# Optimization experiments

Hardware: AMD Instinct MI355X
Metric: run time of the kernel (lower is better)

The kernel has to match this reference:

```python
import jax, jax.numpy as jnp
import numpy as np

K = 1024
D = 64
BETA = 0.25
EPS = 1e-10


def setup_inputs() -> dict:
    key = jax.random.key(0)
    k1, k2 = jax.random.split(key)
    z = jax.random.normal(k1, (64, D, 32, 32), dtype=jnp.float32)
    # embedding.weight.data.uniform_(-1/K, 1/K)
    emb = jax.random.uniform(k2, (K, D), dtype=jnp.float32,
                             minval=-1.0 / K, maxval=1.0 / K)
    return {"z": z, "emb": emb}


def reference(z, emb):
    sg = jax.lax.stop_gradient
    B, C, H, W = z.shape  # C == D
    zp = jnp.transpose(z, (0, 2, 3, 1))            # [B,H,W,D]
    zf = zp.reshape(-1, C)                          # [N,D]
    # squared-euclidean distances via matmul (cdist expansion)
    d = (jnp.sum(zf ** 2, axis=1, keepdims=True)
         + jnp.sum(emb ** 2, axis=1)
         - 2.0 * jnp.matmul(zf, emb.T))             # [N,K]
    idx = jnp.argmin(d, axis=1)                     # [N] int
    z_q = emb[idx].reshape(zp.shape)                # gather == one-hot matmul
    loss = (jnp.mean((sg(z_q) - zp) ** 2)
            + BETA * jnp.mean((z_q - sg(zp)) ** 2))
    # straight-through estimator
    z_q_st = zp + sg(z_q - zp)
    # codebook usage perplexity
    n = zf.shape[0]
    e_mean = jnp.zeros((K,), dtype=zf.dtype).at[idx].add(1.0) / n
    perplexity = jnp.exp(-jnp.sum(e_mean * jnp.log(e_mean + EPS)))
    z_q_out = jnp.transpose(z_q_st, (0, 3, 1, 2))   # back to [B,D,H,W]
    return (loss, z_q_out, perplexity, idx.reshape(B, H, W))
```

## Files before the change

kernel.cpp:

```cpp
#include <hip/hip_runtime.h>
#include <hip/hip_bf16.h>

typedef __attribute__((ext_vector_type(8)))  short short8;
typedef __attribute__((ext_vector_type(16))) float f32x16;

#define NVEC 65536
#define KC   1024
#define DD   64

#define OUT_ZQ   1
#define OUT_PPL  4194305
#define OUT_IDX  4194306

#define SC_SZ    0
#define SC_SN    65536
#define SC_FBL   131072

#define WS_FILT  0
#define WS_HIST  131072
#define WS_SUMSQ 135168
#define WS_FBCNT 135176
#define WS_SE    135184
#define WS_EBFH  139280
#define WS_EBFL  270352
#define WS_EMBT  401424

__global__ __launch_bounds__(256) void prep_z(const float* __restrict__ z,
                                              float* __restrict__ sz,
                                              float* __restrict__ snv) {
    const int n  = blockIdx.x * 256 + threadIdx.x;
    const int b  = n >> 10;
    const int hw = n & 1023;
    const float* zp = z + (size_t)b * 65536 + hw;
    float r[8];
    float sa = 0.0f;
    #pragma unroll
    for (int c = 0; c < 64; ++c) {
        float v = zp[(size_t)c * 1024];
        float s = __fmul_rn(v, v);
        if (c < 8) r[c] = s;
        else       r[c & 7] = __fadd_rn(r[c & 7], s);
        sa += fabsf(v);
    }
    sz[n] = __fadd_rn(__fadd_rn(__fadd_rn(r[0], r[1]), __fadd_rn(r[2], r[3])),
                      __fadd_rn(__fadd_rn(r[4], r[5]), __fadd_rn(r[6], r[7])));
    snv[n] = sa;
}

__global__ __launch_bounds__(256) void prep_emb(const float* __restrict__ emb,
                                                float* __restrict__ se,
                                                unsigned short* __restrict__ ebfh,
                                                unsigned short* __restrict__ ebfl,
                                                float* __restrict__ embT) {
    __shared__ float tile[64][65];
    const int tid = threadIdx.x;
    const int k0  = blockIdx.x * 64;
    {
        const int r = tid >> 2, q = tid & 3;
        const float* row = emb + (size_t)(k0 + r) * 64 + q * 16;
        #pragma unroll
        for (int i = 0; i < 4; ++i) {
            float4 v = *(const float4*)(row + i * 4);
            tile[r][q * 16 + i * 4 + 0] = v.x;
            tile[r][q * 16 + i * 4 + 1] = v.y;
            tile[r][q * 16 + i * 4 + 2] = v.z;
            tile[r][q * 16 + i * 4 + 3] = v.w;
        }
    }
    __syncthreads();
    if (tid < 64) {
        float r[8];
        #pragma unroll
        for (int c = 0; c < 64; ++c) {
            float v = tile[tid][c];
            float s = __fmul_rn(v, v);
            if (c < 8) r[c] = s;
            else       r[c & 7] = __fadd_rn(r[c & 7], s);
        }
        se[k0 + tid] = __fadd_rn(
            __fadd_rn(__fadd_rn(r[0], r[1]), __fadd_rn(r[2], r[3])),
            __fadd_rn(__fadd_rn(r[4], r[5]), __fadd_rn(r[6], r[7])));
    }
    const int kl = tid & 63, cg = tid >> 6;
    #pragma unroll
    for (int i = 0; i < 16; ++i) {
        int c = cg * 16 + i;
        embT[(size_t)c * KC + k0 + kl] = tile[kl][c];
    }
    unsigned* ebh32 = (unsigned*)ebfh;
    unsigned* ebl32 = (unsigned*)ebfl;
    #pragma unroll
    for (int pp = 0; pp < 8; ++pp) {
        int p  = cg * 16 + pp * 2;
        int s  = p >> 4, rem = p & 15;
        int q  = rem >> 3, h = (rem >> 2) & 1, j = rem & 3;
        int c0 = s * 16 + 8 * h + 4 * q + j;
        float v0 = tile[kl][c0], v1 = tile[kl][c0 + 1];
        __hip_bfloat16 h0 = __float2bfloat16(v0);
        __hip_bfloat16 h1 = __float2bfloat16(v1);
        float r0 = v0 - __bfloat162float(h0);
        float r1 = v1 - __bfloat162float(h1);
        __hip_bfloat16 l0 = __float2bfloat16(r0);
        __hip_bfloat16 l1 = __float2bfloat16(r1);
        unsigned uh0 = *(unsigned short*)&h0, uh1 = *(unsigned short*)&h1;
        unsigned ul0 = *(unsigned short*)&l0, ul1 = *(unsigned short*)&l1;
        size_t widx = ((size_t)(k0 + kl) * 64 + p) >> 1;
        ebh32[widx] = uh0 | (uh1 << 16);
        ebl32[widx] = ul0 | (ul1 << 16);
    }
}

__global__ __launch_bounds__(256)
void phase1(const float* __restrict__ z,
            const unsigned short* __restrict__ ebfh,
            const unsigned short* __restrict__ ebfl,
            const float* __restrict__ se,
            const float* __restrict__ snv,
            unsigned short* __restrict__ filt,
            unsigned* __restrict__ fbcnt,
            unsigned* __restrict__ fblist) {
    __shared__ float    sK1d[4][64][16];
    __shared__ float    sK2d[4][64][16];
    __shared__ unsigned sK1k[4][64][16];

    const int tid = threadIdx.x;
    const int w   = tid >> 6;
    const int l   = tid & 63;
    const int q   = l >> 5;
    const int col = l & 31;
    const int nwave = blockIdx.x * 128 + w * 32;

    const int nA = nwave + col;
    const int bA = nA >> 10, hwA = nA & 1023;
    short8 afh[4], afl[4];
    #pragma unroll
    for (int s = 0; s < 4; ++s)
        #pragma unroll
        for (int h = 0; h < 2; ++h)
            #pragma unroll
            for (int j = 0; j < 4; ++j) {
                int c = s * 16 + 8 * h + 4 * q + j;
                float v = z[(size_t)bA * 65536 + (size_t)c * 1024 + hwA];
                __hip_bfloat16 bh = __float2bfloat16(v);
                float rv = v - __bfloat162float(bh);
                __hip_bfloat16 bl = __float2bfloat16(rv);
                afh[s][4 * h + j] = *(short*)&bh;
                afl[s][4 * h + j] = *(short*)&bl;
            }

    float K1d[16], K2d[16]; unsigned K1k[16];
    #pragma unroll
    for (int r = 0; r < 16; ++r) { K1d[r] = K2d[r] = __builtin_inff(); K1k[r] = 0; }

    for (int t = 0; t < 32; ++t) {
        const int kcur = t * 32 + col;
        const unsigned short* ebh = ebfh + (size_t)kcur * 64 + q * 8;
        const unsigned short* ebl = ebfl + (size_t)kcur * 64 + q * 8;
        short8 bh0 = *(const short8*)(ebh + 0);
        short8 bh1 = *(const short8*)(ebh + 16);
        short8 bh2 = *(const short8*)(ebh + 32);
        short8 bh3 = *(const short8*)(ebh + 48);
        short8 bl0 = *(const short8*)(ebl + 0);
        short8 bl1 = *(const short8*)(ebl + 16);
        short8 bl2 = *(const short8*)(ebl + 32);
        short8 bl3 = *(const short8*)(ebl + 48);
        const float sek = se[kcur];
        f32x16 acc;
        #pragma unroll
        for (int r = 0; r < 16; ++r) acc[r] = 0.0f;
        acc = __builtin_amdgcn_mfma_f32_32x32x16_bf16(afh[0], bh0, acc, 0, 0, 0);
        acc = __builtin_amdgcn_mfma_f32_32x32x16_bf16(afl[0], bh0, acc, 0, 0, 0);
        acc = __builtin_amdgcn_mfma_f32_32x32x16_bf16(afh[0], bl0, acc, 0, 0, 0);
        acc = __builtin_amdgcn_mfma_f32_32x32x16_bf16(afh[1], bh1, acc, 0, 0, 0);
        acc = __builtin_amdgcn_mfma_f32_32x32x16_bf16(afl[1], bh1, acc, 0, 0, 0);
        acc = __builtin_amdgcn_mfma_f32_32x32x16_bf16(afh[1], bl1, acc, 0, 0, 0);
        acc = __builtin_amdgcn_mfma_f32_32x32x16_bf16(afh[2], bh2, acc, 0, 0, 0);
        acc = __builtin_amdgcn_mfma_f32_32x32x16_bf16(afl[2], bh2, acc, 0, 0, 0);
        acc = __builtin_amdgcn_mfma_f32_32x32x16_bf16(afh[2], bl2, acc, 0, 0, 0);
        acc = __builtin_amdgcn_mfma_f32_32x32x16_bf16(afh[3], bh3, acc, 0, 0, 0);
        acc = __builtin_amdgcn_mfma_f32_32x32x16_bf16(afl[3], bh3, acc, 0, 0, 0);
        acc = __builtin_amdgcn_mfma_f32_32x32x16_bf16(afh[3], bl3, acc, 0, 0, 0);
        #pragma unroll
        for (int r = 0; r < 16; ++r) {
            float d = __fmaf_rn(-2.0f, acc[r], sek);
            bool c1 = d < K1d[r];
            bool c2 = d < K2d[r];
            K2d[r] = c1 ? K1d[r] : (c2 ? d : K2d[r]);
            K1k[r] = c1 ? (unsigned)kcur : K1k[r];
            K1d[r] = c1 ? d : K1d[r];
        }
    }

    #pragma unroll
    for (int r = 0; r < 16; ++r) {
        sK1d[w][l][r] = K1d[r];
        sK2d[w][l][r] = K2d[r];
        sK1k[w][l][r] = K1k[r];
    }
    __syncthreads();

    if (l < 32) {
        const int o = l;
        const int n = nwave + o;
        const int h = (o >> 2) & 1;
        const int s = (o & 3) + 4 * (o >> 3);
        float b1 = __builtin_inff(), b2 = __builtin_inff();
        unsigned bk = 0;
        for (int j = 0; j < 32; ++j) {
            float d = sK1d[w][h * 32 + j][s];
            unsigned kk = sK1k[w][h * 32 + j][s];
            bool better = (d < b1) || (d == b1 && kk < bk);
            if (better) { b2 = b1; b1 = d; bk = kk; }
            else        b2 = fminf(b2, d);
        }
        for (int j = 0; j < 32; ++j)
            b2 = fminf(b2, sK2d[w][h * 32 + j][s]);
        float margin = __fmaf_rn(snv[n], 2.0e-7f, 6.0e-5f);
        filt[n] = (unsigned short)bk;
        if (b2 <= b1 + margin) {
            unsigned pos = atomicAdd(fbcnt, 1u);
            fblist[pos] = (unsigned)n;
        }
    }
}

__global__ __launch_bounds__(256)
void fallback_kernel(const float* __restrict__ z,
                     const float* __restrict__ embT,
                     const float* __restrict__ se,
                     const float* __restrict__ sz,
                     const unsigned int* __restrict__ fbcnt,
                     const unsigned int* __restrict__ fblist,
                     unsigned short* __restrict__ filt) {
    const int tid = threadIdx.x;
    const int w = tid >> 6, l = tid & 63;
    const unsigned total = *fbcnt;
    for (unsigned i = blockIdx.x * 4 + w; i < total; i += gridDim.x * 4) {
        const int n = (int)fblist[i];
        const int b = n >> 10, hw = n & 1023;
        float zl = z[(size_t)b * 65536 + (size_t)l * 1024 + hw];
        float acc[16];
        #pragma unroll
        for (int p = 0; p < 16; ++p) acc[p] = 0.0f;
        for (int c = 0; c < 64; ++c) {
            float zc = __shfl(zl, c, 64);
            const float* eb = embT + (size_t)c * KC + l;
            #pragma unroll
            for (int p = 0; p < 16; ++p)
                acc[p] = __fmaf_rn(zc, eb[p * 64], acc[p]);
        }
        const float szn = sz[n];
        unsigned long long best = 0xFFFFFFFFFFFFFFFFULL;
        #pragma unroll
        for (int p = 0; p < 16; ++p) {
            int kp = l + p * 64;
            float d = __fmaf_rn(-2.0f, acc[p], __fadd_rn(szn, se[kp]));
            unsigned m = __float_as_uint(d);
            m ^= ((int)m < 0) ? 0xFFFFFFFFu : 0x80000000u;
            unsigned long long key =
                ((unsigned long long)m << 10) | (unsigned)kp;
            best = key < best ? key : best;
        }
        #pragma unroll
        for (int off = 32; off; off >>= 1) {
            unsigned long long o = __shfl_xor(best, off, 64);
            best = o < best ? o : best;
        }
        if (l == 0) filt[n] = (unsigned short)(best & 1023ULL);
    }
}

__global__ __launch_bounds__(256) void zq_kernel(const float* __restrict__ z,
                                                 const float* __restrict__ emb,
                                                 const unsigned short* __restrict__ filt,
                                                 float* __restrict__ out,
                                                 int* __restrict__ hist,
                                                 double* __restrict__ sumsq) {
    __shared__ double red[256];
    const int tid = threadIdx.x;
    const int n   = blockIdx.x * 256 + tid;
    const int b   = n >> 10;
    const int hw  = n & 1023;
    const int idx = (int)filt[n] & 1023;

    out[OUT_IDX + n] = (float)idx;
    atomicAdd(&hist[idx], 1);

    const float* zp = z   + (size_t)b * 65536 + hw;
    float*       op = out + OUT_ZQ + (size_t)b * 65536 + hw;
    const float* er = emb + (size_t)idx * DD;
    double s = 0.0;
    #pragma unroll
    for (int c = 0; c < DD; ++c) {
        float zv   = zp[(size_t)c * 1024];
        float ev   = er[c];
        float diff = ev - zv;
        op[(size_t)c * 1024] = zv + diff;
        s = fma((double)diff, (double)diff, s);
    }
    red[tid] = s;
    __syncthreads();
    for (int off = 128; off > 0; off >>= 1) {
        if (tid < off) red[tid] += red[tid + off];
        __syncthreads();
    }
    if (tid == 0) atomicAdd(sumsq, red[0]);
}

__global__ __launch_bounds__(256) void final_kernel(const int* __restrict__ hist,
                                                    const double* __restrict__ sumsq,
                                                    float* __restrict__ out) {
    __shared__ double red[256];
    const int tid = threadIdx.x;
    double s = 0.0;
    #pragma unroll
    for (int j = 0; j < 4; ++j) {
        int   kk = j * 256 + tid;
        float em = (float)hist[kk] * (1.0f / 65536.0f);
        float t  = em * logf(em + 1e-10f);
        s += (double)t;
    }
    red[tid] = s;
    __syncthreads();
    for (int off = 128; off > 0; off >>= 1) {
        if (tid < off) red[tid] += red[tid + off];
        __syncthreads();
    }
    if (tid == 0) {
        out[OUT_PPL] = expf(-(float)red[0]);
        out[0]       = 1.25f * (float)(sumsq[0] / 4194304.0);
    }
}

extern "C" void kernel_launch(void* const* d_in, const int* in_sizes, int n_in,
                              void* d_out, int out_size, void* d_ws, size_t ws_size,
                              hipStream_t stream) {
    const float* z   = (const float*)d_in[0];
    const float* emb = (const float*)d_in[1];
    float* out = (float*)d_out;
    char*  ws  = (char*)d_ws;

    unsigned short* filt  = (unsigned short*)(ws + WS_FILT);
    int*            hist  = (int*)(ws + WS_HIST);
    double*         sumsq = (double*)(ws + WS_SUMSQ);
    unsigned*       fbcnt = (unsigned*)(ws + WS_FBCNT);
    float*          se    = (float*)(ws + WS_SE);
    unsigned short* ebfh  = (unsigned short*)(ws + WS_EBFH);
    unsigned short* ebfl  = (unsigned short*)(ws + WS_EBFL);
    float*          embT  = (float*)(ws + WS_EMBT);

    float*    zscr   = out + OUT_ZQ;
    float*    sz     = zscr + SC_SZ;
    float*    snv    = zscr + SC_SN;
    unsigned* fblist = (unsigned*)(zscr + SC_FBL);

    hipMemsetAsync(ws + WS_HIST, 0, 4112, stream);

    prep_z  <<<NVEC / 256, 256, 0, stream>>>(z, sz, snv);
    prep_emb<<<KC / 64,    256, 0, stream>>>(emb, se, ebfh, ebfl, embT);
    phase1  <<<NVEC / 128, 256, 0, stream>>>(z, ebfh, ebfl, se, snv,
                                             filt, fbcnt, fblist);
    fallback_kernel<<<128, 256, 0, stream>>>(z, embT, se, sz, fbcnt, fblist, filt);
    zq_kernel      <<<NVEC / 256, 256, 0, stream>>>(z, emb, filt, out, hist, sumsq);
    final_kernel   <<<1, 256, 0, stream>>>(hist, sumsq, out);
}
```

Measured before the change: 161.6 us.

## Split codebook across grid.y in distance kernel and merge top-2 in new kernel

The nearest-code search kernel now splits the 1024 codes into 4 chunks over a second grid dimension, so four times as many blocks run. Each block writes per-chunk best distance, index and second-best to scratch in the output buffer, and a new merge kernel combines them and does the fallback flagging. The shared-memory cross-lane reduction is replaced by xor shuffles. The three MFMA chains are split into independent accumulators to break the serial dependency. The cost is recomputing the bf16 split of z in every chunk, extra global scratch traffic and one more launch.

After: 191.8 us. 18.7% more time.

```diff
diff --git a/kernel.cpp b/kernel.cpp
--- a/kernel.cpp
+++ b/kernel.cpp
@@ -7,6 +7,7 @@
 #define NVEC 65536
 #define KC   1024
 #define DD   64
+#define KSPLIT 4
 
 #define OUT_ZQ   1
 #define OUT_PPL  4194305
@@ -15,6 +16,9 @@
 #define SC_SZ    0
 #define SC_SN    65536
 #define SC_FBL   131072
+#define SC_RD1   196608
+#define SC_RK1   458752
+#define SC_RD2   720896
 
 #define WS_FILT  0
 #define WS_HIST  131072
@@ -115,20 +119,16 @@
             const unsigned short* __restrict__ ebfh,
             const unsigned short* __restrict__ ebfl,
             const float* __restrict__ se,
-            const float* __restrict__ snv,
-            unsigned short* __restrict__ filt,
-            unsigned* __restrict__ fbcnt,
-            unsigned* __restrict__ fblist) {
-    __shared__ float    sK1d[4][64][16];
-    __shared__ float    sK2d[4][64][16];
-    __shared__ unsigned sK1k[4][64][16];
-
+            float* __restrict__ rd1,
+            unsigned* __restrict__ rk1,
+            float* __restrict__ rd2) {
     const int tid = threadIdx.x;
     const int w   = tid >> 6;
     const int l   = tid & 63;
     const int q   = l >> 5;
     const int col = l & 31;
     const int nwave = blockIdx.x * 128 + w * 32;
+    const int kbase = blockIdx.y * (KC / KSPLIT);
 
     const int nA = nwave + col;
     const int bA = nA >> 10, hwA = nA & 1023;
@@ -152,8 +152,8 @@
     #pragma unroll
     for (int r = 0; r < 16; ++r) { K1d[r] = K2d[r] = __builtin_inff(); K1k[r] = 0; }
 
-    for (int t = 0; t < 32; ++t) {
-        const int kcur = t * 32 + col;
+    for (int t = 0; t < (KC / KSPLIT) / 32; ++t) {
+        const int kcur = kbase + t * 32 + col;
         const unsigned short* ebh = ebfh + (size_t)kcur * 64 + q * 8;
         const unsigned short* ebl = ebfl + (size_t)kcur * 64 + q * 8;
         short8 bh0 = *(const short8*)(ebh + 0);
@@ -165,24 +165,26 @@
         short8 bl2 = *(const short8*)(ebl + 32);
         short8 bl3 = *(const short8*)(ebl + 48);
         const float sek = se[kcur];
-        f32x16 acc;
-        #pragma unroll
-        for (int r = 0; r < 16; ++r) acc[r] = 0.0f;
-        acc = __builtin_amdgcn_mfma_f32_32x32x16_bf16(afh[0], bh0, acc, 0, 0, 0);
-        acc = __builtin_amdgcn_mfma_f32_32x32x16_bf16(afl[0], bh0, acc, 0, 0, 0);
-        acc = __builtin_amdgcn_mfma_f32_32x32x16_bf16(afh[0], bl0, acc, 0, 0, 0);
-        acc = __builtin_amdgcn_mfma_f32_32x32x16_bf16(afh[1], bh1, acc, 0, 0, 0);
-        acc = __builtin_amdgcn_mfma_f32_32x32x16_bf16(afl[1], bh1, acc, 0, 0, 0);
-        acc = __builtin_amdgcn_mfma_f32_32x32x16_bf16(afh[1], bl1, acc, 0, 0, 0);
-        acc = __builtin_amdgcn_mfma_f32_32x32x16_bf16(afh[2], bh2, acc, 0, 0, 0);
-        acc = __builtin_amdgcn_mfma_f32_32x32x16_bf16(afl[2], bh2, acc, 0, 0, 0);
-        acc = __builtin_amdgcn_mfma_f32_32x32x16_bf16(afh[2], bl2, acc, 0, 0, 0);
-        acc = __builtin_amdgcn_mfma_f32_32x32x16_bf16(afh[3], bh3, acc, 0, 0, 0);
-        acc = __builtin_amdgcn_mfma_f32_32x32x16_bf16(afl[3], bh3, acc, 0, 0, 0);
-        acc = __builtin_amdgcn_mfma_f32_32x32x16_bf16(afh[3], bl3, acc, 0, 0, 0);
+        f32x16 aA, aB, aC;
+        #pragma unroll
+        for (int r = 0; r < 16; ++r) { aA[r] = 0.0f; aB[r] = 0.0f; aC[r] = 0.0f; }
+        aA = __builtin_amdgcn_mfma_f32_32x32x16_bf16(afh[0], bh0, aA, 0, 0, 0);
+        aB = __builtin_amdgcn_mfma_f32_32x32x16_bf16(afl[0], bh0, aB, 0, 0, 0);
+        aC = __builtin_amdgcn_mfma_f32_32x32x16_bf16(afh[0], bl0, aC, 0, 0, 0);
+        aA = __builtin_amdgcn_mfma_f32_32x32x16_bf16(afh[1], bh1, aA, 0, 0, 0);
+        aB = __builtin_amdgcn_mfma_f32_32x32x16_bf16(afl[1], bh1, aB, 0, 0, 0);
+        aC = __builtin_amdgcn_mfma_f32_32x32x16_bf16(afh[1], bl1, aC, 0, 0, 0);
+        aA = __builtin_amdgcn_mfma_f32_32x32x16_bf16(afh[2], bh2, aA, 0, 0, 0);
+        aB = __builtin_amdgcn_mfma_f32_32x32x16_bf16(afl[2], bh2, aB, 0, 0, 0);
+        aC = __builtin_amdgcn_mfma_f32_32x32x16_bf16(afh[2], bl2, aC, 0, 0, 0);
+        aA = __builtin_amdgcn_mfma_f32_32x32x16_bf16(afh[3], bh3, aA, 0, 0, 0);
+        aB = __builtin_amdgcn_mfma_f32_32x32x16_bf16(afl[3], bh3, aB, 0, 0, 0);
+        aC = __builtin_amdgcn_mfma_f32_32x32x16_bf16(afh[3], bl3, aC, 0, 0, 0);
         #pragma unroll
         for (int r = 0; r < 16; ++r) {
-            float d = __fmaf_rn(-2.0f, acc[r], sek);
+            float d = __fmaf_rn(-2.0f, aC[r],
+                      __fmaf_rn(-2.0f, aB[r],
+                      __fmaf_rn(-2.0f, aA[r], sek)));
             bool c1 = d < K1d[r];
             bool c2 = d < K2d[r];
             K2d[r] = c1 ? K1d[r] : (c2 ? d : K2d[r]);
@@ -191,36 +193,61 @@
         }
     }
 
+    const size_t roff = (size_t)blockIdx.y * NVEC;
     #pragma unroll
     for (int r = 0; r < 16; ++r) {
-        sK1d[w][l][r] = K1d[r];
-        sK2d[w][l][r] = K2d[r];
-        sK1k[w][l][r] = K1k[r];
-    }
-    __syncthreads();
-
-    if (l < 32) {
-        const int o = l;
-        const int n = nwave + o;
-        const int h = (o >> 2) & 1;
-        const int s = (o & 3) + 4 * (o >> 3);
-        float b1 = __builtin_inff(), b2 = __builtin_inff();
-        unsigned bk = 0;
-        for (int j = 0; j < 32; ++j) {
-            float d = sK1d[w][h * 32 + j][s];
-            unsigned kk = sK1k[w][h * 32 + j][s];
-            bool better = (d < b1) || (d == b1 && kk < bk);
-            if (better) { b2 = b1; b1 = d; bk = kk; }
-            else        b2 = fminf(b2, d);
-        }
-        for (int j = 0; j < 32; ++j)
-            b2 = fminf(b2, sK2d[w][h * 32 + j][s]);
-        float margin = __fmaf_rn(snv[n], 2.0e-7f, 6.0e-5f);
-        filt[n] = (unsigned short)bk;
-        if (b2 <= b1 + margin) {
-            unsigned pos = atomicAdd(fbcnt, 1u);
-            fblist[pos] = (unsigned)n;
-        }
+        float    d1 = K1d[r];
+        unsigned k1 = K1k[r];
+        float    d2 = K2d[r];
+        #pragma unroll
+        for (int off = 1; off < 32; off <<= 1) {
+            float    od1 = __shfl_xor(d1, off, 64);
+            unsigned ok1 = (unsigned)__shfl_xor((int)k1, off, 64);
+            float    od2 = __shfl_xor(d2, off, 64);
+            bool better = (od1 < d1) || (od1 == d1 && ok1 < k1);
+            float loser = better ? d1 : od1;
+            d2 = fminf(fminf(d2, od2), loser);
+            d1 = better ? od1 : d1;
+            k1 = better ? ok1 : k1;
+        }
+        if ((l & 31) == 0) {
+            int row = (r & 3) + 8 * (r >> 2) + 4 * q;
+            int n   = nwave + row;
+            rd1[roff + n] = d1;
+            rk1[roff + n] = k1;
+            rd2[roff + n] = d2;
+        }
+    }
+}
+
+__global__ __launch_bounds__(256)
+void merge_kernel(const float* __restrict__ rd1,
+                  const unsigned* __restrict__ rk1,
+                  const float* __restrict__ rd2,
+                  const float* __restrict__ snv,
+                  unsigned short* __restrict__ filt,
+                  unsigned* __restrict__ fbcnt,
+                  unsigned* __restrict__ fblist) {
+    const int n = blockIdx.x * 256 + threadIdx.x;
+    float bd = __builtin_inff(); unsigned bk = 0; int br = 0;
+    #pragma unroll
+    for (int r = 0; r < KSPLIT; ++r) {
+        float    d = rd1[(size_t)r * NVEC + n];
+        unsigned k = rk1[(size_t)r * NVEC + n];
+        bool better = (d < bd) || (d == bd && k < bk);
+        if (better) { bd = d; bk = k; br = r; }
+    }
+    float b2 = __builtin_inff();
+    #pragma unroll
+    for (int r = 0; r < KSPLIT; ++r) {
+        b2 = fminf(b2, rd2[(size_t)r * NVEC + n]);
+        if (r != br) b2 = fminf(b2, rd1[(size_t)r * NVEC + n]);
+    }
+    float margin = __fmaf_rn(snv[n], 2.0e-7f, 6.0e-5f);
+    filt[n] = (unsigned short)bk;
+    if (b2 <= bd + margin) {
+        unsigned pos = atomicAdd(fbcnt, 1u);
+        fblist[pos] = (unsigned)n;
     }
 }
 
@@ -353,13 +380,18 @@
     float*    sz     = zscr + SC_SZ;
     float*    snv    = zscr + SC_SN;
     unsigned* fblist = (unsigned*)(zscr + SC_FBL);
+    float*    rd1    = zscr + SC_RD1;
+    unsigned* rk1    = (unsigned*)(zscr + SC_RK1);
+    float*    rd2    = zscr + SC_RD2;
 
     hipMemsetAsync(ws + WS_HIST, 0, 4112, stream);
 
     prep_z  <<<NVEC / 256, 256, 0, stream>>>(z, sz, snv);
     prep_emb<<<KC / 64,    256, 0, stream>>>(emb, se, ebfh, ebfl, embT);
-    phase1  <<<NVEC / 128, 256, 0, stream>>>(z, ebfh, ebfl, se, snv,
-                                             filt, fbcnt, fblist);
+    phase1  <<<dim3(NVEC / 128, KSPLIT), 256, 0, stream>>>(z, ebfh, ebfl, se,
+                                                           rd1, rk1, rd2);
+    merge_kernel<<<NVEC / 256, 256, 0, stream>>>(rd1, rk1, rd2, snv,
+                                                 filt, fbcnt, fblist);
     fallback_kernel<<<128, 256, 0, stream>>>(z, embT, se, sz, fbcnt, fblist, filt);
     zq_kernel      <<<NVEC / 256, 256, 0, stream>>>(z, emb, filt, out, hist, sumsq);
     final_kernel   <<<1, 256, 0, stream>>>(hist, sumsq, out);
```
